# Kernel optimization log

Hardware: AMD Instinct MI355X
Metric: run time of the kernel (lower is better)

## Reference

```python
import jax, jax.numpy as jnp
import numpy as np

FEATURE_IN = 4096
FEATURE_OUT = 4096
R = 16
ALPHA = 32.0


def setup_inputs() -> dict:
    key = jax.random.key(0)
    k_x, k_w, k_b, k_a = jax.random.split(key, 4)
    x = jax.random.normal(k_x, (4, 2048, FEATURE_IN), dtype=jnp.float32)
    # base linear (torch nn.Linear): weight [out, in], bias [out]
    bound = 1.0 / np.sqrt(FEATURE_IN)
    w = jax.random.uniform(k_w, (FEATURE_OUT, FEATURE_IN), dtype=jnp.float32, minval=-bound, maxval=bound)
    b = jax.random.uniform(k_b, (FEATURE_OUT,), dtype=jnp.float32, minval=-bound, maxval=bound)
    # lora_a: kaiming uniform over [feature_in, r]; lora_b: zeros -> use small randn so grads are nontrivial? No: faithful init is zeros, but zeros makes LoRA path trivially zero. Use kaiming for a, small random for b to exercise the math.
    gain = np.sqrt(2.0 / (1.0 + 5.0 ** 2))  # kaiming_uniform default a=sqrt(5)
    bound_a = gain * np.sqrt(3.0 / FEATURE_IN)
    lora_a = jax.random.uniform(k_a, (FEATURE_IN, R), dtype=jnp.float32, minval=-bound_a, maxval=bound_a)
    lora_b = jax.random.normal(jax.random.fold_in(key, 7), (R, FEATURE_OUT), dtype=jnp.float32) * 0.01
    return {"x": x, "w": w, "b": b, "lora_a": lora_a, "lora_b": lora_b}


def reference(x, w, b, lora_a, lora_b):
    # base linear: x @ W^T + b
    output1 = jnp.einsum('bsi,oi->bso', x, w) + b
    # faithful to source: materialize (A @ B) [feature_in, feature_out] first,
    # then x @ (A@B), scaled by alpha/r
    ab = jnp.matmul(lora_a, lora_b)  # [feature_in, feature_out]
    output2 = jnp.matmul(x, ab) * (ALPHA / R)
    return output2 + output1
```

## Files before the change

kernel.cpp:

```cpp
#include <hip/hip_runtime.h>
#include <cstdint>
#include <cstddef>

#define FEATURE_IN 4096
#define FEATURE_OUT 4096
#define RNK 16

typedef __bf16 bf16x8_t __attribute__((ext_vector_type(8)));
typedef __bf16 bf16x4_t __attribute__((ext_vector_type(4)));
typedef float f32x4_t __attribute__((ext_vector_type(4)));

#define FW_KB 128
#define FW_NB 32
#define NFUSE 4096
#define NCVTB 2048
#define CVT_THREADS (NCVTB * 256)
#define CVT_CHUNKS 16

__global__ __launch_bounds__(256) void prep_all(const float* __restrict__ x,
                                                uint16_t* __restrict__ xb,
                                                const float* __restrict__ w,
                                                const float* __restrict__ la,
                                                const float* __restrict__ lb,
                                                uint16_t* __restrict__ wf) {
    __shared__ float las[FW_KB * RNK];
    __shared__ float lbs[RNK * FW_NB];

    const int tid = threadIdx.x;

    if (blockIdx.x >= NFUSE) {
        const int tg = (blockIdx.x - NFUSE) * 256 + tid;
        const float4* xp = (const float4*)x;
        bf16x4_t* op = (bf16x4_t*)xb;
#pragma unroll
        for (int i = 0; i < CVT_CHUNKS; ++i) {
            const int idx = i * CVT_THREADS + tg;
            float4 v = xp[idx];
            bf16x4_t o;
            o[0] = (__bf16)v.x; o[1] = (__bf16)v.y; o[2] = (__bf16)v.z; o[3] = (__bf16)v.w;
            op[idx] = o;
        }
        return;
    }

    const int bid = blockIdx.x;
    const int kb = (bid & 31) * FW_KB;
    const int nb = (bid >> 5) * FW_NB;

    {
        const float4* src = (const float4*)(la + (size_t)kb * RNK);
        float4* dst = (float4*)las;
        dst[tid] = src[tid];
        dst[tid + 256] = src[tid + 256];
    }
#pragma unroll
    for (int f = tid; f < RNK * FW_NB; f += 256) {
        int r = f >> 5;
        int nl = f & 31;
        lbs[r * FW_NB + nl] = lb[(size_t)r * FEATURE_OUT + nb + nl];
    }
    __syncthreads();

    const int nl = tid >> 3;
    const int kq = tid & 7;

    f32x4_t bcol[4];
#pragma unroll
    for (int r4 = 0; r4 < 4; ++r4) {
        f32x4_t v;
#pragma unroll
        for (int j = 0; j < 4; ++j) v[j] = lbs[(r4 * 4 + j) * FW_NB + nl];
        bcol[r4] = v;
    }

    const f32x4_t* las4 = (const f32x4_t*)las;
    const float* wrow = w + (size_t)(nb + nl) * FEATURE_IN + kb + kq * 16;
    uint16_t* wfrow = wf + (size_t)(nb + nl) * FEATURE_IN + kb + kq * 16;

#pragma unroll
    for (int h = 0; h < 2; ++h) {
        float4 wv0 = ((const float4*)wrow)[h * 2 + 0];
        float4 wv1 = ((const float4*)wrow)[h * 2 + 1];
        float wfv[8] = {wv0.x, wv0.y, wv0.z, wv0.w, wv1.x, wv1.y, wv1.z, wv1.w};
        bf16x8_t o;
#pragma unroll
        for (int j = 0; j < 8; ++j) {
            const int k = kq * 16 + h * 8 + j;
            float s = 0.f;
#pragma unroll
            for (int rr = 0; rr < 4; ++rr) {
                const int r4 = (rr + kq) & 3;
                f32x4_t av = las4[k * 4 + r4];
                f32x4_t bv = bcol[r4];
                s += av[0] * bv[0] + av[1] * bv[1] + av[2] * bv[2] + av[3] * bv[3];
            }
            o[j] = (__bf16)(wfv[j] + 2.f * s);
        }
        ((bf16x8_t*)wfrow)[h] = o;
    }
}

#define BM 256
#define BN 256
#define BK 32
#define NT (FEATURE_IN / BK)

#define ABUF(b) ((b) * 32768)
#define BBUF(b) ((b) * 32768 + 16384)

#define MFMA16X(S) do { _Pragma("unroll")                                                \
    for (int _mi = 0; _mi < 4; ++_mi) { _Pragma("unroll")                                \
        for (int _ni = 0; _ni < 4; ++_ni)                                                \
            acc[_mi][_ni] = __builtin_amdgcn_mfma_f32_16x16x32_bf16(                     \
                afx[S][_mi], bqr[S][_ni], acc[_mi][_ni], 0, 0, 0); } } while (0)

#define MFMA16Y(S) do { _Pragma("unroll")                                                \
    for (int _mi = 0; _mi < 4; ++_mi) { _Pragma("unroll")                                \
        for (int _ni = 0; _ni < 4; ++_ni)                                                \
            acc[4 + _mi][_ni] = __builtin_amdgcn_mfma_f32_16x16x32_bf16(                 \
                afy[_mi], bqr[S][_ni], acc[4 + _mi][_ni], 0, 0, 0); } } while (0)

#define READ_AFY(b) do { _Pragma("unroll")                                               \
    for (int _mi = 0; _mi < 4; ++_mi)                                                    \
        afy[_mi] = *(const bf16x8_t*)(lds + ABUF(b) + aoff[4 + _mi]); } while (0)

#define READ_R0(b, SN) do { _Pragma("unroll")                                            \
    for (int _mi = 0; _mi < 4; ++_mi)                                                    \
        afx[SN][_mi] = *(const bf16x8_t*)(lds + ABUF(b) + aoff[_mi]);                    \
    _Pragma("unroll")                                                                    \
    for (int _ni = 0; _ni < 4; ++_ni)                                                    \
        bqr[SN][_ni] = *(const bf16x8_t*)(lds + BBUF(b) + boff[_ni]); } while (0)

#define GLL(SRC, DSTOFF)                                                                 \
    __builtin_amdgcn_global_load_lds(                                                    \
        (const __attribute__((address_space(1))) void*)(SRC),                            \
        (__attribute__((address_space(3))) void*)(lds + (DSTOFF) + wv * 1024), 16, 0, 0)

#define STAGE_A(b) do { GLL(pA0, ABUF(b)); GLL(pA1, ABUF(b) + 8192); } while (0)
#define STAGE_B(b) do { GLL(pB0, BBUF(b)); GLL(pB1, BBUF(b) + 8192); } while (0)

#define PBAR() __builtin_amdgcn_s_barrier()
#define PRIO1 __builtin_amdgcn_s_setprio(1)
#define PRIO0 __builtin_amdgcn_s_setprio(0)
#define VMCNT(n) asm volatile("s_waitcnt vmcnt(" #n ")" ::: "memory")
#define SCHEDB() __builtin_amdgcn_sched_barrier(0)

#define TILE_BODY(CUR, NXT, S, SN)                                                       \
    READ_AFY(CUR);                                                                       \
    STAGE_A(NXT);                                                                        \
    SCHEDB();                                                                            \
    PRIO1; MFMA16X(S); PRIO0;                                                            \
    VMCNT(6);                                                                            \
    PBAR();                                                                              \
    READ_R0((CUR + 1) & 3, SN);                                                          \
    STAGE_B(NXT);                                                                        \
    SCHEDB();                                                                            \
    PRIO1; MFMA16Y(S); PRIO0;                                                            \
    PBAR();                                                                              \
    pA0 += BK; pA1 += BK; pB0 += BK; pB1 += BK;

#define TAIL_BODY(CUR, S, SN, NWAIT)                                                     \
    READ_AFY(CUR);                                                                       \
    SCHEDB();                                                                            \
    PRIO1; MFMA16X(S); PRIO0;                                                            \
    VMCNT(NWAIT);                                                                        \
    PBAR();                                                                              \
    READ_R0((CUR + 1) & 3, SN);                                                          \
    SCHEDB();                                                                            \
    PRIO1; MFMA16Y(S); PRIO0;                                                            \
    PBAR();

__global__ __launch_bounds__(512, 2) void gemm256(const uint16_t* __restrict__ Au,
                                                  const uint16_t* __restrict__ Bu,
                                                  const float* __restrict__ bias,
                                                  float* __restrict__ C,
                                                  int M, int N, int K) {
    __shared__ __align__(16) char lds[131072];

    const __bf16* A = (const __bf16*)Au;
    const __bf16* B = (const __bf16*)Bu;

    const int tid  = threadIdx.x;
    const int wv   = tid >> 6;
    const int lane = tid & 63;
    const int waveM = wv >> 2;
    const int waveN = wv & 3;
    const int l15 = lane & 15;
    const int q   = lane >> 4;

    const int nbx = N / BN;
    const int nwg = nbx * (M / BM);
    const int bidlin = blockIdx.y * nbx + blockIdx.x;
    const int swz = (bidlin & 7) * (nwg >> 3) + (bidlin >> 3);
    const int by = swz / nbx;
    const int bx = swz - by * nbx;
    const int m0 = by * BM;
    const int n0 = bx * BN;

    const int srow = tid >> 2;
    const int sq   = ((tid & 3) - (srow >> 1)) & 3;
    const __bf16* pA0 = A + (size_t)(m0 + srow) * K + sq * 8;
    const __bf16* pA1 = pA0 + (size_t)128 * K;
    const __bf16* pB0 = B + (size_t)(n0 + srow) * K + sq * 8;
    const __bf16* pB1 = pB0 + (size_t)128 * K;

    int aoff[8], boff[4];
#pragma unroll
    for (int mi = 0; mi < 8; ++mi) {
        int row = waveM * 128 + mi * 16 + l15;
        aoff[mi] = row * 64 + (((row >> 1) + q) & 3) * 16;
    }
#pragma unroll
    for (int ni = 0; ni < 4; ++ni) {
        int row = waveN * 64 + ni * 16 + l15;
        boff[ni] = row * 64 + (((row >> 1) + q) & 3) * 16;
    }

    f32x4_t acc[8][4];
#pragma unroll
    for (int mi = 0; mi < 8; ++mi)
#pragma unroll
        for (int ni = 0; ni < 4; ++ni)
            acc[mi][ni] = (f32x4_t)0.f;

    bf16x8_t afx[2][4], afy[4], bqr[2][4];

    STAGE_A(0); STAGE_B(0); pA0 += BK; pA1 += BK; pB0 += BK; pB1 += BK;
    STAGE_A(1); STAGE_B(1); pA0 += BK; pA1 += BK; pB0 += BK; pB1 += BK;
    STAGE_A(2); STAGE_B(2); pA0 += BK; pA1 += BK; pB0 += BK; pB1 += BK;
    VMCNT(8);
    PBAR();
    READ_R0(0, 0);

#pragma unroll 1
    for (int i = 0; i < 31; ++i) {
        TILE_BODY(0, 3, 0, 1)
        TILE_BODY(1, 0, 1, 0)
        TILE_BODY(2, 1, 0, 1)
        TILE_BODY(3, 2, 1, 0)
    }
    TILE_BODY(0, 3, 0, 1)

    TAIL_BODY(1, 1, 0, 4)
    TAIL_BODY(2, 0, 1, 0)
    READ_AFY(3);
    SCHEDB();
    PRIO1; MFMA16X(1); PRIO0;
    PRIO1; MFMA16Y(1); PRIO0;

#pragma unroll
    for (int ni = 0; ni < 4; ++ni) {
        const int col = n0 + waveN * 64 + ni * 16 + l15;
        const float bv = bias[col];
#pragma unroll
        for (int mi = 0; mi < 8; ++mi) {
            const int row = m0 + waveM * 128 + mi * 16 + q * 4;
            float* op = C + (size_t)row * N + col;
#pragma unroll
            for (int j = 0; j < 4; ++j)
                op[(size_t)j * N] = acc[mi][ni][j] + bv;
        }
    }
}

extern "C" void kernel_launch(void* const* d_in, const int* in_sizes, int n_in,
                              void* d_out, int out_size, void* d_ws, size_t ws_size,
                              hipStream_t stream) {
    const float* x  = (const float*)d_in[0];
    const float* w  = (const float*)d_in[1];
    const float* b  = (const float*)d_in[2];
    const float* la = (const float*)d_in[3];
    const float* lb = (const float*)d_in[4];
    float* out = (float*)d_out;

    const int M = in_sizes[0] / FEATURE_IN;
    const int K = FEATURE_IN;
    const int N = FEATURE_OUT;

    uint16_t* xb = (uint16_t*)d_ws;
    uint16_t* wf = (uint16_t*)((char*)d_ws + (size_t)M * K * 2);

    prep_all<<<NFUSE + NCVTB, 256, 0, stream>>>(x, xb, w, la, lb, wf);

    {
        dim3 grid(N / BN, M / BM);
        gemm256<<<grid, 512, 0, stream>>>(xb, wf, b, out, M, N, K);
    }
}
```

Measured before the change: 509.0 us.

## Replace merged-weight LoRA with low-rank extra K-tile and in-GEMM fp32 weight conversion

The prep pass no longer builds a merged bf16 weight W + 2·A·B. A small GEMM now computes x·A (scaled by 2) into a padded rank-32 buffer, and B is transposed and padded. The main GEMM appends one extra K tile carrying the low-rank product. It also loads fp32 W directly, converting it to bf16 in registers before writing to LDS, so the separate weight-conversion pass and its workspace traffic go away. The cost is that W staging shifts from async global_load_lds to register loads with vmcnt(0) waits each tile, and the B operand pipeline shrinks from three tiles ahead to one. That may expose memory latency in the main loop.

```diff
diff --git a/kernel.cpp b/kernel.cpp
--- a/kernel.cpp
+++ b/kernel.cpp
@@ -10,100 +10,128 @@
 typedef __bf16 bf16x4_t __attribute__((ext_vector_type(4)));
 typedef float f32x4_t __attribute__((ext_vector_type(4)));
 
-#define FW_KB 128
-#define FW_NB 32
-#define NFUSE 4096
-#define NCVTB 2048
-#define CVT_THREADS (NCVTB * 256)
-#define CVT_CHUNKS 16
-
-__global__ __launch_bounds__(256) void prep_all(const float* __restrict__ x,
-                                                uint16_t* __restrict__ xb,
-                                                const float* __restrict__ w,
-                                                const float* __restrict__ la,
-                                                const float* __restrict__ lb,
-                                                uint16_t* __restrict__ wf) {
-    __shared__ float las[FW_KB * RNK];
-    __shared__ float lbs[RNK * FW_NB];
-
+typedef const __attribute__((address_space(1))) f32x4_t* gf4p;
+typedef const __attribute__((address_space(1))) bf16x8_t* gb8p;
+
+__global__ __launch_bounds__(256) void prep1(const float* __restrict__ x,
+                                             uint16_t* __restrict__ xb,
+                                             const float* __restrict__ la,
+                                             const float* __restrict__ lb,
+                                             uint16_t* __restrict__ labT,
+                                             uint16_t* __restrict__ be) {
     const int tid = threadIdx.x;
-
-    if (blockIdx.x >= NFUSE) {
-        const int tg = (blockIdx.x - NFUSE) * 256 + tid;
-        const float4* xp = (const float4*)x;
-        bf16x4_t* op = (bf16x4_t*)xb;
-#pragma unroll
-        for (int i = 0; i < CVT_CHUNKS; ++i) {
-            const int idx = i * CVT_THREADS + tg;
-            float4 v = xp[idx];
-            bf16x4_t o;
-            o[0] = (__bf16)v.x; o[1] = (__bf16)v.y; o[2] = (__bf16)v.z; o[3] = (__bf16)v.w;
-            op[idx] = o;
+    const int bid = blockIdx.x;
+
+    if (bid < 16) {
+        const int r = tid >> 4, kt = tid & 15;
+        const int k0 = bid * 256 + kt * 16;
+        bf16x8_t o0, o1;
+#pragma unroll
+        for (int i = 0; i < 8; ++i) o0[i] = (__bf16)la[(size_t)(k0 + i) * RNK + r];
+#pragma unroll
+        for (int i = 0; i < 8; ++i) o1[i] = (__bf16)la[(size_t)(k0 + 8 + i) * RNK + r];
+        *(bf16x8_t*)(labT + (size_t)r * FEATURE_IN + k0) = o0;
+        *(bf16x8_t*)(labT + (size_t)r * FEATURE_IN + k0 + 8) = o1;
+        return;
+    }
+    if (bid < 32) {
+        const int n = (bid - 16) * 256 + tid;
+        bf16x8_t o0, o1, zz;
+#pragma unroll
+        for (int i = 0; i < 8; ++i) o0[i] = (__bf16)lb[(size_t)i * FEATURE_OUT + n];
+#pragma unroll
+        for (int i = 0; i < 8; ++i) o1[i] = (__bf16)lb[(size_t)(8 + i) * FEATURE_OUT + n];
+#pragma unroll
+        for (int i = 0; i < 8; ++i) zz[i] = (__bf16)0.f;
+        *(bf16x8_t*)(be + (size_t)n * 32) = o0;
+        *(bf16x8_t*)(be + (size_t)n * 32 + 8) = o1;
+        *(bf16x8_t*)(be + (size_t)n * 32 + 16) = zz;
+        *(bf16x8_t*)(be + (size_t)n * 32 + 24) = zz;
+        return;
+    }
+    const int tg = (bid - 32) * 256 + tid;
+    const f32x4_t* xp = (const f32x4_t*)x;
+    bf16x4_t* op = (bf16x4_t*)xb;
+#pragma unroll
+    for (int i = 0; i < 16; ++i) {
+        const int idx = i * 524288 + tg;
+        f32x4_t v = xp[idx];
+        bf16x4_t o;
+        o[0] = (__bf16)v[0]; o[1] = (__bf16)v[1]; o[2] = (__bf16)v[2]; o[3] = (__bf16)v[3];
+        op[idx] = o;
+    }
+}
+
+#define XGLL(SRC, DSTOFF)                                                                \
+    __builtin_amdgcn_global_load_lds(                                                    \
+        (const __attribute__((address_space(1))) void*)(SRC),                            \
+        (__attribute__((address_space(3))) void*)(lds + (DSTOFF) + wv2 * 1024), 16, 0, 0)
+
+__global__ __launch_bounds__(256) void xa_gemm(const uint16_t* __restrict__ xbu,
+                                               const uint16_t* __restrict__ labTu,
+                                               uint16_t* __restrict__ xe) {
+    __shared__ __align__(16) char lds[16384];
+    const __bf16* Xb = (const __bf16*)xbu;
+    const __bf16* Lt = (const __bf16*)labTu;
+
+    const int tid = threadIdx.x;
+    const int wv2 = tid >> 6;
+    const int lane = tid & 63;
+    const int l15 = lane & 15;
+    const int q = lane >> 4;
+    const int m0 = blockIdx.x * 128;
+
+    const int srow = tid >> 2;
+    const int sq = ((tid & 3) - (srow >> 1)) & 3;
+    const __bf16* pX0 = Xb + (size_t)(m0 + srow) * FEATURE_IN + sq * 8;
+    const __bf16* pX1 = pX0 + (size_t)64 * FEATURE_IN;
+
+    int aoff2[2];
+#pragma unroll
+    for (int mi = 0; mi < 2; ++mi) {
+        int row = wv2 * 32 + mi * 16 + l15;
+        aoff2[mi] = row * 64 + (((row >> 1) + q) & 3) * 16;
+    }
+
+    f32x4_t acc2[2];
+    acc2[0] = (f32x4_t)0.f; acc2[1] = (f32x4_t)0.f;
+    bf16x8_t b2[2];
+
+    XGLL(pX0, 0); XGLL(pX1, 4096);
+    pX0 += 32; pX1 += 32;
+    b2[0] = *(gb8p)(Lt + (size_t)l15 * FEATURE_IN + q * 8);
+
+#pragma unroll 2
+    for (int t = 0; t < 128; ++t) {
+        asm volatile("s_waitcnt vmcnt(0)" ::: "memory");
+        __builtin_amdgcn_s_barrier();
+        const int cur = t & 1;
+        bf16x8_t a0 = *(const bf16x8_t*)(lds + cur * 8192 + aoff2[0]);
+        bf16x8_t a1 = *(const bf16x8_t*)(lds + cur * 8192 + aoff2[1]);
+        if (t < 127) {
+            const int nxt = cur ^ 1;
+            XGLL(pX0, nxt * 8192); XGLL(pX1, nxt * 8192 + 4096);
+            pX0 += 32; pX1 += 32;
+            b2[(t + 1) & 1] = *(gb8p)(Lt + (size_t)l15 * FEATURE_IN + (t + 1) * 32 + q * 8);
         }
-        return;
-    }
-
-    const int bid = blockIdx.x;
-    const int kb = (bid & 31) * FW_KB;
-    const int nb = (bid >> 5) * FW_NB;
-
-    {
-        const float4* src = (const float4*)(la + (size_t)kb * RNK);
-        float4* dst = (float4*)las;
-        dst[tid] = src[tid];
-        dst[tid + 256] = src[tid + 256];
-    }
-#pragma unroll
-    for (int f = tid; f < RNK * FW_NB; f += 256) {
-        int r = f >> 5;
-        int nl = f & 31;
-        lbs[r * FW_NB + nl] = lb[(size_t)r * FEATURE_OUT + nb + nl];
-    }
-    __syncthreads();
-
-    const int nl = tid >> 3;
-    const int kq = tid & 7;
-
-    f32x4_t bcol[4];
-#pragma unroll
-    for (int r4 = 0; r4 < 4; ++r4) {
-        f32x4_t v;
-#pragma unroll
-        for (int j = 0; j < 4; ++j) v[j] = lbs[(r4 * 4 + j) * FW_NB + nl];
-        bcol[r4] = v;
-    }
-
-    const f32x4_t* las4 = (const f32x4_t*)las;
-    const float* wrow = w + (size_t)(nb + nl) * FEATURE_IN + kb + kq * 16;
-    uint16_t* wfrow = wf + (size_t)(nb + nl) * FEATURE_IN + kb + kq * 16;
-
-#pragma unroll
-    for (int h = 0; h < 2; ++h) {
-        float4 wv0 = ((const float4*)wrow)[h * 2 + 0];
-        float4 wv1 = ((const float4*)wrow)[h * 2 + 1];
-        float wfv[8] = {wv0.x, wv0.y, wv0.z, wv0.w, wv1.x, wv1.y, wv1.z, wv1.w};
-        bf16x8_t o;
-#pragma unroll
-        for (int j = 0; j < 8; ++j) {
-            const int k = kq * 16 + h * 8 + j;
-            float s = 0.f;
-#pragma unroll
-            for (int rr = 0; rr < 4; ++rr) {
-                const int r4 = (rr + kq) & 3;
-                f32x4_t av = las4[k * 4 + r4];
-                f32x4_t bv = bcol[r4];
-                s += av[0] * bv[0] + av[1] * bv[1] + av[2] * bv[2] + av[3] * bv[3];
-            }
-            o[j] = (__bf16)(wfv[j] + 2.f * s);
+        acc2[0] = __builtin_amdgcn_mfma_f32_16x16x32_bf16(a0, b2[cur], acc2[0], 0, 0, 0);
+        acc2[1] = __builtin_amdgcn_mfma_f32_16x16x32_bf16(a1, b2[cur], acc2[1], 0, 0, 0);
+    }
+
+    __bf16* xeb = (__bf16*)xe;
+#pragma unroll
+    for (int mi = 0; mi < 2; ++mi)
+#pragma unroll
+        for (int j = 0; j < 4; ++j) {
+            const int row = m0 + wv2 * 32 + mi * 16 + q * 4 + j;
+            xeb[(size_t)row * 32 + l15] = (__bf16)(2.f * acc2[mi][j]);
+            xeb[(size_t)row * 32 + 16 + l15] = (__bf16)0.f;
         }
-        ((bf16x8_t*)wfrow)[h] = o;
-    }
 }
 
 #define BM 256
 #define BN 256
 #define BK 32
-#define NT (FEATURE_IN / BK)
 
 #define ABUF(b) ((b) * 32768)
 #define BBUF(b) ((b) * 32768 + 16384)
@@ -112,7 +140,7 @@
     for (int _mi = 0; _mi < 4; ++_mi) { _Pragma("unroll")                                \
         for (int _ni = 0; _ni < 4; ++_ni)                                                \
             acc[_mi][_ni] = __builtin_amdgcn_mfma_f32_16x16x32_bf16(                     \
-                afx[S][_mi], bqr[S][_ni], acc[_mi][_ni], 0, 0, 0); } } while (0)
+                afx[_mi], bqr[S][_ni], acc[_mi][_ni], 0, 0, 0); } } while (0)
 
 #define MFMA16Y(S) do { _Pragma("unroll")                                                \
     for (int _mi = 0; _mi < 4; ++_mi) { _Pragma("unroll")                                \
@@ -126,7 +154,7 @@
 
 #define READ_R0(b, SN) do { _Pragma("unroll")                                            \
     for (int _mi = 0; _mi < 4; ++_mi)                                                    \
-        afx[SN][_mi] = *(const bf16x8_t*)(lds + ABUF(b) + aoff[_mi]);                    \
+        afx[_mi] = *(const bf16x8_t*)(lds + ABUF(b) + aoff[_mi]);                        \
     _Pragma("unroll")                                                                    \
     for (int _ni = 0; _ni < 4; ++_ni)                                                    \
         bqr[SN][_ni] = *(const bf16x8_t*)(lds + BBUF(b) + boff[_ni]); } while (0)
@@ -136,49 +164,62 @@
         (const __attribute__((address_space(1))) void*)(SRC),                            \
         (__attribute__((address_space(3))) void*)(lds + (DSTOFF) + wv * 1024), 16, 0, 0)
 
-#define STAGE_A(b) do { GLL(pA0, ABUF(b)); GLL(pA1, ABUF(b) + 8192); } while (0)
-#define STAGE_B(b) do { GLL(pB0, BBUF(b)); GLL(pB1, BBUF(b) + 8192); } while (0)
+#define STAGE_A(b) do { GLL(pA0, ABUF(b)); GLL(pA1, ABUF(b) + 8192);                     \
+                        pA0 += BK; pA1 += BK; } while (0)
+
+#define BLD_W() do {                                                                     \
+    wba0 = *(gf4p)(pW0);     wba1 = *(gf4p)(pW0 + 4);                                    \
+    wbb0 = *(gf4p)(pW1);     wbb1 = *(gf4p)(pW1 + 4);                                    \
+    pW0 += BK; pW1 += BK; } while (0)
+
+#define BWR_W(BUFI) do {                                                                 \
+    bf16x8_t _o0, _o1;                                                                   \
+    _o0[0] = (__bf16)wba0[0]; _o0[1] = (__bf16)wba0[1];                                  \
+    _o0[2] = (__bf16)wba0[2]; _o0[3] = (__bf16)wba0[3];                                  \
+    _o0[4] = (__bf16)wba1[0]; _o0[5] = (__bf16)wba1[1];                                  \
+    _o0[6] = (__bf16)wba1[2]; _o0[7] = (__bf16)wba1[3];                                  \
+    _o1[0] = (__bf16)wbb0[0]; _o1[1] = (__bf16)wbb0[1];                                  \
+    _o1[2] = (__bf16)wbb0[2]; _o1[3] = (__bf16)wbb0[3];                                  \
+    _o1[4] = (__bf16)wbb1[0]; _o1[5] = (__bf16)wbb1[1];                                  \
+    _o1[6] = (__bf16)wbb1[2]; _o1[7] = (__bf16)wbb1[3];                                  \
+    *(bf16x8_t*)(lds + BBUF(BUFI) + bwOff) = _o0;                                        \
+    *(bf16x8_t*)(lds + BBUF(BUFI) + 8192 + bwOff) = _o1; } while (0)
 
 #define PBAR() __builtin_amdgcn_s_barrier()
 #define PRIO1 __builtin_amdgcn_s_setprio(1)
 #define PRIO0 __builtin_amdgcn_s_setprio(0)
-#define VMCNT(n) asm volatile("s_waitcnt vmcnt(" #n ")" ::: "memory")
+#define VMCNT0() asm volatile("s_waitcnt vmcnt(0)" ::: "memory")
+#define LGKM0() asm volatile("s_waitcnt lgkmcnt(0)" ::: "memory")
 #define SCHEDB() __builtin_amdgcn_sched_barrier(0)
 
-#define TILE_BODY(CUR, NXT, S, SN)                                                       \
+#define BODYF(CUR, S, SN)                                                                \
+    VMCNT0();                                                                            \
+    BWR_W((CUR + 1) & 3);                                                                \
     READ_AFY(CUR);                                                                       \
-    STAGE_A(NXT);                                                                        \
+    STAGE_A((CUR + 2) & 3);                                                              \
+    BLD_W();                                                                             \
     SCHEDB();                                                                            \
     PRIO1; MFMA16X(S); PRIO0;                                                            \
-    VMCNT(6);                                                                            \
-    PBAR();                                                                              \
-    READ_R0((CUR + 1) & 3, SN);                                                          \
-    STAGE_B(NXT);                                                                        \
     SCHEDB();                                                                            \
-    PRIO1; MFMA16Y(S); PRIO0;                                                            \
-    PBAR();                                                                              \
-    pA0 += BK; pA1 += BK; pB0 += BK; pB1 += BK;
-
-#define TAIL_BODY(CUR, S, SN, NWAIT)                                                     \
-    READ_AFY(CUR);                                                                       \
-    SCHEDB();                                                                            \
-    PRIO1; MFMA16X(S); PRIO0;                                                            \
-    VMCNT(NWAIT);                                                                        \
+    LGKM0();                                                                             \
     PBAR();                                                                              \
     READ_R0((CUR + 1) & 3, SN);                                                          \
     SCHEDB();                                                                            \
     PRIO1; MFMA16Y(S); PRIO0;                                                            \
-    PBAR();
-
-__global__ __launch_bounds__(512, 2) void gemm256(const uint16_t* __restrict__ Au,
-                                                  const uint16_t* __restrict__ Bu,
-                                                  const float* __restrict__ bias,
-                                                  float* __restrict__ C,
-                                                  int M, int N, int K) {
+    SCHEDB();
+
+__global__ __launch_bounds__(512, 2) void gemm256f(const uint16_t* __restrict__ Au,
+                                                   const float* __restrict__ W,
+                                                   const uint16_t* __restrict__ xeu,
+                                                   const uint16_t* __restrict__ beu,
+                                                   const float* __restrict__ bias,
+                                                   float* __restrict__ C,
+                                                   int M, int N, int K) {
     __shared__ __align__(16) char lds[131072];
 
     const __bf16* A = (const __bf16*)Au;
-    const __bf16* B = (const __bf16*)Bu;
+    const __bf16* XE = (const __bf16*)xeu;
+    const __bf16* BE = (const __bf16*)beu;
 
     const int tid  = threadIdx.x;
     const int wv   = tid >> 6;
@@ -199,10 +240,15 @@
 
     const int srow = tid >> 2;
     const int sq   = ((tid & 3) - (srow >> 1)) & 3;
+    const int bwOff = srow * 64 + (tid & 3) * 16;
     const __bf16* pA0 = A + (size_t)(m0 + srow) * K + sq * 8;
     const __bf16* pA1 = pA0 + (size_t)128 * K;
-    const __bf16* pB0 = B + (size_t)(n0 + srow) * K + sq * 8;
-    const __bf16* pB1 = pB0 + (size_t)128 * K;
+    const float* pW0 = W + (size_t)(n0 + srow) * K + sq * 8;
+    const float* pW1 = pW0 + (size_t)128 * K;
+    const __bf16* pAe0 = XE + (size_t)(m0 + srow) * 32 + sq * 8;
+    const __bf16* pAe1 = pAe0 + (size_t)128 * 32;
+    const __bf16* pBe0 = BE + (size_t)(n0 + srow) * 32 + sq * 8;
+    const __bf16* pBe1 = pBe0 + (size_t)128 * 32;
 
     int aoff[8], boff[4];
 #pragma unroll
@@ -223,30 +269,65 @@
         for (int ni = 0; ni < 4; ++ni)
             acc[mi][ni] = (f32x4_t)0.f;
 
-    bf16x8_t afx[2][4], afy[4], bqr[2][4];
-
-    STAGE_A(0); STAGE_B(0); pA0 += BK; pA1 += BK; pB0 += BK; pB1 += BK;
-    STAGE_A(1); STAGE_B(1); pA0 += BK; pA1 += BK; pB0 += BK; pB1 += BK;
-    STAGE_A(2); STAGE_B(2); pA0 += BK; pA1 += BK; pB0 += BK; pB1 += BK;
-    VMCNT(8);
+    bf16x8_t afx[4], afy[4], bqr[2][4];
+    f32x4_t wba0, wba1, wbb0, wbb1;
+
+    STAGE_A(0);
+    BLD_W();
+    VMCNT0();
+    BWR_W(0);
+    STAGE_A(1);
+    BLD_W();
+    LGKM0();
     PBAR();
     READ_R0(0, 0);
 
 #pragma unroll 1
     for (int i = 0; i < 31; ++i) {
-        TILE_BODY(0, 3, 0, 1)
-        TILE_BODY(1, 0, 1, 0)
-        TILE_BODY(2, 1, 0, 1)
-        TILE_BODY(3, 2, 1, 0)
-    }
-    TILE_BODY(0, 3, 0, 1)
-
-    TAIL_BODY(1, 1, 0, 4)
-    TAIL_BODY(2, 0, 1, 0)
+        BODYF(0, 0, 1)
+        BODYF(1, 1, 0)
+        BODYF(2, 0, 1)
+        BODYF(3, 1, 0)
+    }
+    BODYF(0, 0, 1)
+    BODYF(1, 1, 0)
+
+    VMCNT0();
+    BWR_W(3);
+    READ_AFY(2);
+    GLL(pAe0, ABUF(0)); GLL(pAe1, ABUF(0) + 8192);
+    SCHEDB();
+    PRIO1; MFMA16X(0); PRIO0;
+    SCHEDB();
+    LGKM0();
+    PBAR();
+    READ_R0(3, 1);
+    SCHEDB();
+    PRIO1; MFMA16Y(0); PRIO0;
+    SCHEDB();
+
+    VMCNT0();
+    {
+        bf16x8_t e0 = *(gb8p)(pBe0);
+        bf16x8_t e1 = *(gb8p)(pBe1);
+        VMCNT0();
+        *(bf16x8_t*)(lds + BBUF(0) + bwOff) = e0;
+        *(bf16x8_t*)(lds + BBUF(0) + 8192 + bwOff) = e1;
+    }
     READ_AFY(3);
     SCHEDB();
     PRIO1; MFMA16X(1); PRIO0;
+    SCHEDB();
+    LGKM0();
+    PBAR();
+    READ_R0(0, 0);
+    SCHEDB();
     PRIO1; MFMA16Y(1); PRIO0;
+    SCHEDB();
+
+    READ_AFY(0);
+    SCHEDB();
+    PRIO1; MFMA16X(0); MFMA16Y(0); PRIO0;
 
 #pragma unroll
     for (int ni = 0; ni < 4; ++ni) {
@@ -277,13 +358,17 @@
     const int K = FEATURE_IN;
     const int N = FEATURE_OUT;
 
-    uint16_t* xb = (uint16_t*)d_ws;
-    uint16_t* wf = (uint16_t*)((char*)d_ws + (size_t)M * K * 2);
-
-    prep_all<<<NFUSE + NCVTB, 256, 0, stream>>>(x, xb, w, la, lb, wf);
+    uint16_t* xb   = (uint16_t*)d_ws;
+    uint16_t* labT = xb + (size_t)M * K;
+    uint16_t* be   = labT + (size_t)RNK * K;
+    uint16_t* xe   = be + (size_t)N * 32;
+
+    prep1<<<2080, 256, 0, stream>>>(x, xb, la, lb, labT, be);
+
+    xa_gemm<<<64, 256, 0, stream>>>(xb, labT, xe);
 
     {
         dim3 grid(N / BN, M / BM);
-        gemm256<<<grid, 512, 0, stream>>>(xb, wf, b, out, M, N, K);
+        gemm256f<<<grid, 512, 0, stream>>>(xb, w, xe, be, b, out, M, N, K);
     }
 }
```

Result: slower. 879.9 us (+72.9%).

## Restructure GEMM main loop to one barrier per K-tile with merged staging

Applied to the files above, without the earlier changes.

The 4-stage LDS pipeline loop body drops from two barriers per K-tile to one. All A and B global-to-LDS loads for the next stage are issued together right after the single barrier, and an explicit lgkmcnt(0) wait is added before it. The A fragment double-buffer becomes single-buffered, which cuts register use. The aim is less barrier stall per iteration; the risks are less overlap of LDS reads with MFMAs and a possible WAR hazard on the buffer being restaged. The x-conversion code switches from float4 to a vector type, which is cosmetic.

```diff
diff --git a/kernel.cpp b/kernel.cpp
--- a/kernel.cpp
+++ b/kernel.cpp
@@ -30,14 +30,15 @@
 
     if (blockIdx.x >= NFUSE) {
         const int tg = (blockIdx.x - NFUSE) * 256 + tid;
-        const float4* xp = (const float4*)x;
+        const f32x4_t* xp = (const f32x4_t*)x;
         bf16x4_t* op = (bf16x4_t*)xb;
 #pragma unroll
         for (int i = 0; i < CVT_CHUNKS; ++i) {
             const int idx = i * CVT_THREADS + tg;
-            float4 v = xp[idx];
+            f32x4_t v = xp[idx];
             bf16x4_t o;
-            o[0] = (__bf16)v.x; o[1] = (__bf16)v.y; o[2] = (__bf16)v.z; o[3] = (__bf16)v.w;
+            o[0] = (__bf16)v[0]; o[1] = (__bf16)v[1];
+            o[2] = (__bf16)v[2]; o[3] = (__bf16)v[3];
             op[idx] = o;
         }
         return;
@@ -112,7 +113,7 @@
     for (int _mi = 0; _mi < 4; ++_mi) { _Pragma("unroll")                                \
         for (int _ni = 0; _ni < 4; ++_ni)                                                \
             acc[_mi][_ni] = __builtin_amdgcn_mfma_f32_16x16x32_bf16(                     \
-                afx[S][_mi], bqr[S][_ni], acc[_mi][_ni], 0, 0, 0); } } while (0)
+                afx[_mi], bqr[S][_ni], acc[_mi][_ni], 0, 0, 0); } } while (0)
 
 #define MFMA16Y(S) do { _Pragma("unroll")                                                \
     for (int _mi = 0; _mi < 4; ++_mi) { _Pragma("unroll")                                \
@@ -126,7 +127,7 @@
 
 #define READ_R0(b, SN) do { _Pragma("unroll")                                            \
     for (int _mi = 0; _mi < 4; ++_mi)                                                    \
-        afx[SN][_mi] = *(const bf16x8_t*)(lds + ABUF(b) + aoff[_mi]);                    \
+        afx[_mi] = *(const bf16x8_t*)(lds + ABUF(b) + aoff[_mi]);                        \
     _Pragma("unroll")                                                                    \
     for (int _ni = 0; _ni < 4; ++_ni)                                                    \
         bqr[SN][_ni] = *(const bf16x8_t*)(lds + BBUF(b) + boff[_ni]); } while (0)
@@ -136,39 +137,40 @@
         (const __attribute__((address_space(1))) void*)(SRC),                            \
         (__attribute__((address_space(3))) void*)(lds + (DSTOFF) + wv * 1024), 16, 0, 0)
 
-#define STAGE_A(b) do { GLL(pA0, ABUF(b)); GLL(pA1, ABUF(b) + 8192); } while (0)
-#define STAGE_B(b) do { GLL(pB0, BBUF(b)); GLL(pB1, BBUF(b) + 8192); } while (0)
+#define STAGE_AB(b) do {                                                                 \
+    GLL(pA0, ABUF(b)); GLL(pA1, ABUF(b) + 8192);                                         \
+    GLL(pB0, BBUF(b)); GLL(pB1, BBUF(b) + 8192);                                         \
+    pA0 += BK; pA1 += BK; pB0 += BK; pB1 += BK; } while (0)
 
 #define PBAR() __builtin_amdgcn_s_barrier()
 #define PRIO1 __builtin_amdgcn_s_setprio(1)
 #define PRIO0 __builtin_amdgcn_s_setprio(0)
 #define VMCNT(n) asm volatile("s_waitcnt vmcnt(" #n ")" ::: "memory")
+#define LGKM0() asm volatile("s_waitcnt lgkmcnt(0)" ::: "memory")
 #define SCHEDB() __builtin_amdgcn_sched_barrier(0)
 
-#define TILE_BODY(CUR, NXT, S, SN)                                                       \
-    READ_AFY(CUR);                                                                       \
-    STAGE_A(NXT);                                                                        \
+#define BODY(B, S)                                                                       \
+    READ_AFY(B);                                                                         \
     SCHEDB();                                                                            \
     PRIO1; MFMA16X(S); PRIO0;                                                            \
-    VMCNT(6);                                                                            \
+    VMCNT(4);                                                                            \
+    LGKM0();                                                                             \
     PBAR();                                                                              \
-    READ_R0((CUR + 1) & 3, SN);                                                          \
-    STAGE_B(NXT);                                                                        \
-    SCHEDB();                                                                            \
-    PRIO1; MFMA16Y(S); PRIO0;                                                            \
-    PBAR();                                                                              \
-    pA0 += BK; pA1 += BK; pB0 += BK; pB1 += BK;
-
-#define TAIL_BODY(CUR, S, SN, NWAIT)                                                     \
-    READ_AFY(CUR);                                                                       \
+    STAGE_AB((B + 3) & 3);                                                               \
+    READ_R0((B + 1) & 3, (S) ^ 1);                                                       \
+    SCHEDB();                                                                            \
+    PRIO1; MFMA16Y(S); PRIO0;
+
+#define TAILB(B, S, NWAIT)                                                               \
+    READ_AFY(B);                                                                         \
     SCHEDB();                                                                            \
     PRIO1; MFMA16X(S); PRIO0;                                                            \
     VMCNT(NWAIT);                                                                        \
+    LGKM0();                                                                             \
     PBAR();                                                                              \
-    READ_R0((CUR + 1) & 3, SN);                                                          \
-    SCHEDB();                                                                            \
-    PRIO1; MFMA16Y(S); PRIO0;                                                            \
-    PBAR();
+    READ_R0((B + 1) & 3, (S) ^ 1);                                                       \
+    SCHEDB();                                                                            \
+    PRIO1; MFMA16Y(S); PRIO0;
 
 __global__ __launch_bounds__(512, 2) void gemm256(const uint16_t* __restrict__ Au,
                                                   const uint16_t* __restrict__ Bu,
@@ -223,26 +225,26 @@
         for (int ni = 0; ni < 4; ++ni)
             acc[mi][ni] = (f32x4_t)0.f;
 
-    bf16x8_t afx[2][4], afy[4], bqr[2][4];
-
-    STAGE_A(0); STAGE_B(0); pA0 += BK; pA1 += BK; pB0 += BK; pB1 += BK;
-    STAGE_A(1); STAGE_B(1); pA0 += BK; pA1 += BK; pB0 += BK; pB1 += BK;
-    STAGE_A(2); STAGE_B(2); pA0 += BK; pA1 += BK; pB0 += BK; pB1 += BK;
+    bf16x8_t afx[4], afy[4], bqr[2][4];
+
+    STAGE_AB(0);
+    STAGE_AB(1);
+    STAGE_AB(2);
     VMCNT(8);
     PBAR();
     READ_R0(0, 0);
 
 #pragma unroll 1
     for (int i = 0; i < 31; ++i) {
-        TILE_BODY(0, 3, 0, 1)
-        TILE_BODY(1, 0, 1, 0)
-        TILE_BODY(2, 1, 0, 1)
-        TILE_BODY(3, 2, 1, 0)
-    }
-    TILE_BODY(0, 3, 0, 1)
-
-    TAIL_BODY(1, 1, 0, 4)
-    TAIL_BODY(2, 0, 1, 0)
+        BODY(0, 0)
+        BODY(1, 1)
+        BODY(2, 0)
+        BODY(3, 1)
+    }
+    BODY(0, 0)
+
+    TAILB(1, 1, 4)
+    TAILB(2, 0, 0)
     READ_AFY(3);
     SCHEDB();
     PRIO1; MFMA16X(1); PRIO0;
```

Result: no change. 512.9 us (+0.8%).
